# Optimization experiments

Measured on AMD Instinct MI355X. Metric: run time of the kernel, lower is better.

The kernel has to match this reference:

```python
import jax, jax.numpy as jnp
import numpy as np

N_NODES = 50000
N_EDGES = 800000
F_IN, F_HID, F_OUT = 1433, 64, 32


def setup_inputs() -> dict:
    key = jax.random.key(0)
    ks = jax.random.split(key, 8)
    x = jax.random.normal(ks[0], (N_NODES, F_IN), dtype=jnp.float32)
    edge_index = jax.random.randint(ks[1], (2, N_EDGES), 0, N_NODES, dtype=jnp.int32)
    s1 = 1.0 / np.sqrt(F_IN)
    s2 = 1.0 / np.sqrt(F_HID)
    W1_l = jax.random.normal(ks[2], (F_IN, F_HID), dtype=jnp.float32) * s1
    W1_r = jax.random.normal(ks[3], (F_IN, F_HID), dtype=jnp.float32) * s1
    b1 = jnp.zeros((F_HID,), dtype=jnp.float32)
    W2_l = jax.random.normal(ks[4], (F_HID, F_OUT), dtype=jnp.float32) * s2
    W2_r = jax.random.normal(ks[5], (F_HID, F_OUT), dtype=jnp.float32) * s2
    b2 = jnp.zeros((F_OUT,), dtype=jnp.float32)
    return {"x": x, "edge_index": edge_index, "W1_l": W1_l, "b1": b1,
            "W1_r": W1_r, "W2_l": W2_l, "b2": b2, "W2_r": W2_r}


def sage_conv(x, src, dst, W_l, b_l, W_r, num_nodes):
    # PyG SAGEConv: out = lin_l(mean_{j in N(i)} x_j) + lin_r(x_i)
    # lin_l is linear, so project first then aggregate (saves E x F_in gather).
    msg = x @ W_l                                   # [N, F_out]
    agg = jax.ops.segment_sum(msg[src], dst, num_segments=num_nodes)  # [N, F_out]
    deg = jax.ops.segment_sum(jnp.ones_like(src, dtype=x.dtype), dst,
                              num_segments=num_nodes)                 # [N]
    agg = jnp.where(deg[:, None] > 0, agg / jnp.maximum(deg, 1.0)[:, None], 0.0)
    return agg + b_l + x @ W_r


def reference(x, edge_index, W1_l, b1, W1_r, W2_l, b2, W2_r):
    src, dst = edge_index[0], edge_index[1]
    n = x.shape[0]
    h = sage_conv(x, src, dst, W1_l, b1, W1_r, n)   # [N, 64]  (no activation between convs)
    h = sage_conv(h, src, dst, W2_l, b2, W2_r, n)   # [N, 32]
    h = jax.nn.relu(h)
    # dropout p=0.5 is identity in eval mode
    return jax.nn.log_softmax(h, axis=1)
```

## Files before the change

kernel.cpp:

```cpp
#include <hip/hip_runtime.h>
#include <hip/hip_bf16.h>
#include <cstdint>
#include <cstddef>


#define N_NODES 50000
#define N_EDGES 800000
#define F_IN    1433
#define KP      1472
#define NCH     6
#define DMAX    64

typedef __attribute__((ext_vector_type(8))) short bf16x8;
typedef __attribute__((ext_vector_type(4))) float f32x4;

static constexpr size_t OFF_H1PRE = 0;
static constexpr size_t OFF_H1    = OFF_H1PRE + 25600000;
static constexpr size_t OFF_M2    = OFF_H1    + 12800000;
static constexpr size_t OFF_CUR   = OFF_M2    + 12800000;
static constexpr size_t OFF_ESRC  = OFF_CUR   + 200000;
static constexpr size_t OFF_WT    = OFF_ESRC  + 12800000;

__device__ inline ushort f2bf(float f) {
  union { float f; uint32_t u; } v; v.f = f;
  uint32_t u = v.u + 0x7FFFu + ((v.u >> 16) & 1u);
  return (ushort)(u >> 16);
}

__device__ __forceinline__ void gload_lds16(const void* g, void* l) {
  __builtin_amdgcn_global_load_lds(
      (const __attribute__((address_space(1))) void*)g,
      (__attribute__((address_space(3))) void*)l, 16, 0, 0);
}

__global__ __launch_bounds__(256) void k_zero_cur(int* __restrict__ cur) {
  int i = blockIdx.x * 256 + threadIdx.x;
  if (i < N_NODES) cur[i] = 0;
}

__global__ __launch_bounds__(256) void k_prep_w(const float* __restrict__ Wl,
                                                const float* __restrict__ Wr,
                                                ushort* __restrict__ Wt) {
  const int c = blockIdx.x;
  const int k = blockIdx.y * 256 + threadIdx.x;
  if (k >= KP) return;
  float v = 0.f;
  if (k < F_IN) v = (c < 64) ? Wl[k * 64 + c] : Wr[k * 64 + (c - 64)];
  Wt[(size_t)c * KP + k] = f2bf(v);
}

__global__ __launch_bounds__(256) void k_gemm1c(const float* __restrict__ x,
                                                const ushort* __restrict__ Wt,
                                                float* __restrict__ h1pre) {
  __shared__ __align__(16) ushort As[4][32 * 64];
  __shared__ __align__(16) ushort Bs[4][128 * 64];
  const int t    = threadIdx.x;
  const int lane = t & 63;
  const int w    = t >> 6;
  const int wr   = w >> 1;
  const int wc   = w & 1;
  const int row0 = blockIdx.x * 32;

  const int ar = t >> 3;
  const int aq = t & 7;
  const size_t abase = (size_t)(row0 + ar) * F_IN + aq * 8;
  const size_t LIM   = (size_t)N_NODES * F_IN - 4;
  const int aoff = ar * 64;
  const int asw  = (aq ^ (ar & 7)) * 8;

  const int lr = lane >> 3, lt = lane & 7;
  const ushort* b_src[4];
  ushort* b_dst[4];
#pragma unroll
  for (int j = 0; j < 4; ++j) {
    int r = (w * 4 + j) * 8 + lr;
    b_src[j] = Wt + (size_t)r * KP + (lt ^ (r & 7)) * 8;
    b_dst[j] = (ushort*)&Bs[0][(w * 4 + j) * 512];
  }

  f32x4 acc[4] = {};
  f32x4 av[4][2];

#define LOADA_CHUNK(kbase)                                          \
  do {                                                              \
    _Pragma("unroll")                                               \
    for (int s = 0; s < 4; ++s) {                                   \
      size_t i0 = abase + (size_t)(kbase) + s * 64;                 \
      size_t i1 = i0 + 4;                                           \
      if (i0 > LIM) i0 = LIM;                                       \
      if (i1 > LIM) i1 = LIM;                                       \
      __builtin_memcpy(&av[s][0], x + i0, 16);                      \
      __builtin_memcpy(&av[s][1], x + i1, 16);                      \
    }                                                               \
  } while (0)

  LOADA_CHUNK(0);

  for (int c = 0; c < NCH; ++c) {
    const int kbase = c * 256;
    const int nsub = (c < 5) ? 4 : 3;
#pragma unroll
    for (int s = 0; s < 4; ++s) {
      if (s < nsub) {
        bf16x8 w0;
#pragma unroll
        for (int e = 0; e < 4; ++e) {
          w0[e]     = (short)f2bf(av[s][0][e]);
          w0[4 + e] = (short)f2bf(av[s][1][e]);
        }
        *(bf16x8*)&As[s][aoff + asw] = w0;
      }
    }
#pragma unroll
    for (int s = 0; s < 4; ++s) {
      if (s < nsub) {
#pragma unroll
        for (int j = 0; j < 4; ++j)
          gload_lds16(b_src[j] + kbase + s * 64, b_dst[j] + (size_t)s * (128 * 64));
      }
    }
    __syncthreads();
    if (c + 1 < NCH) LOADA_CHUNK(kbase + 256);
    const int nks = (c < 5) ? 8 : 6;
#pragma unroll
    for (int kk = 0; kk < 8; ++kk) {
      if (kk < nks) {
        const int sub = kk >> 1;
        const int sbase = (kk & 1) * 4 + (lane >> 4);
        bf16x8 a, b[4];
        {
          int r = wr * 16 + (lane & 15);
          int s2 = sbase ^ (r & 7);
          a = *(const bf16x8*)&As[sub][r * 64 + s2 * 8];
        }
#pragma unroll
        for (int n = 0; n < 4; ++n) {
          int r = wc * 64 + n * 16 + (lane & 15);
          int s2 = sbase ^ (r & 7);
          b[n] = *(const bf16x8*)&Bs[sub][r * 64 + s2 * 8];
        }
#pragma unroll
        for (int n = 0; n < 4; ++n)
          acc[n] = __builtin_amdgcn_mfma_f32_16x16x32_bf16(a, b[n], acc[n], 0, 0, 0);
      }
    }
    __syncthreads();
  }
#undef LOADA_CHUNK

  {
    int rbase = row0 + wr * 16 + (lane >> 4) * 4;
#pragma unroll
    for (int n = 0; n < 4; ++n) {
      int col = wc * 64 + n * 16 + (lane & 15);
#pragma unroll
      for (int r = 0; r < 4; ++r) {
        int grow = rbase + r;
        if (grow < N_NODES) h1pre[(size_t)grow * 128 + col] = acc[n][r];
      }
    }
  }
}

__global__ void k_fill_pad(const int* __restrict__ ei, int* __restrict__ cur,
                           int* __restrict__ esrc) {
  int e = blockIdx.x * blockDim.x + threadIdx.x;
  if (e < N_EDGES) {
    int s = ei[e];
    int d = ei[N_EDGES + e];
    int slot = atomicAdd(&cur[d], 1);
    if (slot < DMAX) esrc[(size_t)d * DMAX + slot] = s;
  }
}

__global__ __launch_bounds__(256) void k_agg1(const float* __restrict__ h1pre,
                                              const int* __restrict__ cur,
                                              const int* __restrict__ esrc,
                                              const float* __restrict__ b1,
                                              float* __restrict__ h1) {
  const int lane = threadIdx.x & 63;
  const int d = blockIdx.x * 4 + (threadIdx.x >> 6);
  if (d >= N_NODES) return;
  int dg = cur[d]; if (dg > DMAX) dg = DMAX;
  const size_t base = (size_t)d * DMAX;
  float a0 = 0.f, a1 = 0.f, a2 = 0.f, a3 = 0.f;
  float a4 = 0.f, a5 = 0.f, a6 = 0.f, a7 = 0.f;
  int j = 0;
  for (; j + 8 <= dg; j += 8) {
    int s0 = esrc[base + j],     s1 = esrc[base + j + 1];
    int s2 = esrc[base + j + 2], s3 = esrc[base + j + 3];
    int s4 = esrc[base + j + 4], s5 = esrc[base + j + 5];
    int s6 = esrc[base + j + 6], s7 = esrc[base + j + 7];
    a0 += h1pre[(size_t)s0 * 128 + lane];
    a1 += h1pre[(size_t)s1 * 128 + lane];
    a2 += h1pre[(size_t)s2 * 128 + lane];
    a3 += h1pre[(size_t)s3 * 128 + lane];
    a4 += h1pre[(size_t)s4 * 128 + lane];
    a5 += h1pre[(size_t)s5 * 128 + lane];
    a6 += h1pre[(size_t)s6 * 128 + lane];
    a7 += h1pre[(size_t)s7 * 128 + lane];
  }
  for (; j + 4 <= dg; j += 4) {
    int s0 = esrc[base + j],     s1 = esrc[base + j + 1];
    int s2 = esrc[base + j + 2], s3 = esrc[base + j + 3];
    a0 += h1pre[(size_t)s0 * 128 + lane];
    a1 += h1pre[(size_t)s1 * 128 + lane];
    a2 += h1pre[(size_t)s2 * 128 + lane];
    a3 += h1pre[(size_t)s3 * 128 + lane];
  }
  for (; j < dg; ++j) a0 += h1pre[(size_t)esrc[base + j] * 128 + lane];
  float acc = ((a0 + a1) + (a2 + a3)) + ((a4 + a5) + (a6 + a7));
  const float inv = (dg > 0) ? 1.f / (float)dg : 0.f;
  h1[(size_t)d * 64 + lane] = acc * inv + b1[lane] + h1pre[(size_t)d * 128 + 64 + lane];
}

__global__ __launch_bounds__(256) void k_gemm2(const float* __restrict__ h1,
                                               const float* __restrict__ W2l,
                                               const float* __restrict__ W2r,
                                               float* __restrict__ m2) {
  __shared__ __align__(16) float Ws[64][68];
  __shared__ __align__(16) float Hs[32][68];
  const int t = threadIdx.x;
#pragma unroll
  for (int i = 0; i < 16; ++i) {
    int idx = t + 256 * i;
    int k = idx >> 6, c = idx & 63;
    Ws[k][c] = (c < 32) ? W2l[k * 32 + c] : W2r[k * 32 + (c - 32)];
  }
  const int r0 = blockIdx.x * 32;
#pragma unroll
  for (int i = 0; i < 8; ++i) {
    int idx = t + 256 * i;
    int r = idx >> 6, c = idx & 63;
    int gr = r0 + r;
    Hs[r][c] = (gr < N_NODES) ? h1[(size_t)gr * 64 + c] : 0.f;
  }
  __syncthreads();
  const int rl = t >> 3;
  const int c0 = (t & 7) * 8;
  float acc[8] = {};
#pragma unroll 8
  for (int k = 0; k < 64; ++k) {
    float hv = Hs[rl][k];
#pragma unroll
    for (int j = 0; j < 8; ++j) acc[j] = fmaf(hv, Ws[k][c0 + j], acc[j]);
  }
  const int gr = r0 + rl;
  if (gr < N_NODES) {
    *(float4*)(&m2[(size_t)gr * 64 + c0])     = make_float4(acc[0], acc[1], acc[2], acc[3]);
    *(float4*)(&m2[(size_t)gr * 64 + c0 + 4]) = make_float4(acc[4], acc[5], acc[6], acc[7]);
  }
}

__global__ __launch_bounds__(256) void k_agg2(const float* __restrict__ m2,
                                              const int* __restrict__ cur,
                                              const int* __restrict__ esrc,
                                              const float* __restrict__ b2,
                                              float* __restrict__ out) {
  const int lane = threadIdx.x & 63;
  const int half = lane >> 5;
  const int f = lane & 31;
  const int d = blockIdx.x * 8 + ((threadIdx.x >> 6) << 1) + half;
  int dg = cur[d]; if (dg > DMAX) dg = DMAX;
  const size_t base = (size_t)d * DMAX;
  float a0 = 0.f, a1 = 0.f, a2 = 0.f, a3 = 0.f;
  float a4 = 0.f, a5 = 0.f, a6 = 0.f, a7 = 0.f;
  int j = 0;
  for (; j + 8 <= dg; j += 8) {
    int s0 = esrc[base + j],     s1 = esrc[base + j + 1];
    int s2 = esrc[base + j + 2], s3 = esrc[base + j + 3];
    int s4 = esrc[base + j + 4], s5 = esrc[base + j + 5];
    int s6 = esrc[base + j + 6], s7 = esrc[base + j + 7];
    a0 += m2[(size_t)s0 * 64 + f];
    a1 += m2[(size_t)s1 * 64 + f];
    a2 += m2[(size_t)s2 * 64 + f];
    a3 += m2[(size_t)s3 * 64 + f];
    a4 += m2[(size_t)s4 * 64 + f];
    a5 += m2[(size_t)s5 * 64 + f];
    a6 += m2[(size_t)s6 * 64 + f];
    a7 += m2[(size_t)s7 * 64 + f];
  }
  for (; j + 4 <= dg; j += 4) {
    int s0 = esrc[base + j],     s1 = esrc[base + j + 1];
    int s2 = esrc[base + j + 2], s3 = esrc[base + j + 3];
    a0 += m2[(size_t)s0 * 64 + f];
    a1 += m2[(size_t)s1 * 64 + f];
    a2 += m2[(size_t)s2 * 64 + f];
    a3 += m2[(size_t)s3 * 64 + f];
  }
  for (; j < dg; ++j) a0 += m2[(size_t)esrc[base + j] * 64 + f];
  float acc = ((a0 + a1) + (a2 + a3)) + ((a4 + a5) + (a6 + a7));
  const float inv = (dg > 0) ? 1.f / (float)dg : 0.f;
  float v = acc * inv + b2[f] + m2[(size_t)d * 64 + 32 + f];
  v = fmaxf(v, 0.f);
  float m = v;
#pragma unroll
  for (int o = 16; o > 0; o >>= 1) m = fmaxf(m, __shfl_xor(m, o, 32));
  float e = expf(v - m);
  float sum = e;
#pragma unroll
  for (int o = 16; o > 0; o >>= 1) sum += __shfl_xor(sum, o, 32);
  out[(size_t)d * 32 + f] = v - m - logf(sum);
}

extern "C" void kernel_launch(void* const* d_in, const int* in_sizes, int n_in,
                              void* d_out, int out_size, void* d_ws, size_t ws_size,
                              hipStream_t stream) {
  const float* x   = (const float*)d_in[0];
  const int*   ei  = (const int*)d_in[1];
  const float* W1l = (const float*)d_in[2];
  const float* b1  = (const float*)d_in[3];
  const float* W1r = (const float*)d_in[4];
  const float* W2l = (const float*)d_in[5];
  const float* b2  = (const float*)d_in[6];
  const float* W2r = (const float*)d_in[7];
  float* out = (float*)d_out;

  char* ws = (char*)d_ws;
  float*  h1pre = (float*)(ws + OFF_H1PRE);
  float*  h1    = (float*)(ws + OFF_H1);
  float*  m2    = (float*)(ws + OFF_M2);
  int*    cur   = (int*)(ws + OFF_CUR);
  int*    esrc  = (int*)(ws + OFF_ESRC);
  ushort* Wt    = (ushort*)(ws + OFF_WT);

  k_zero_cur<<<(N_NODES + 255) / 256, 256, 0, stream>>>(cur);

  {
    dim3 g(128, (KP + 255) / 256);
    k_prep_w<<<g, 256, 0, stream>>>(W1l, W1r, Wt);
  }
  k_gemm1c<<<(N_NODES + 31) / 32, 256, 0, stream>>>(x, Wt, h1pre);

  k_fill_pad<<<(N_EDGES + 255) / 256, 256, 0, stream>>>(ei, cur, esrc);

  k_agg1<<<N_NODES / 4, 256, 0, stream>>>(h1pre, cur, esrc, b1, h1);
  k_gemm2<<<(N_NODES + 31) / 32, 256, 0, stream>>>(h1, W2l, W2r, m2);
  k_agg2<<<N_NODES / 8, 256, 0, stream>>>(m2, cur, esrc, b2, out);
}
```

Before: 220.4 us.

## Fuse layer-1 aggregation with layer-2 GEMM via bf16 MFMA; merge init kernels

Result: faster. 203.5 us (-7.7%).

```diff
diff --git a/kernel.cpp b/kernel.cpp
--- a/kernel.cpp
+++ b/kernel.cpp
@@ -15,8 +15,7 @@
 typedef __attribute__((ext_vector_type(4))) float f32x4;
 
 static constexpr size_t OFF_H1PRE = 0;
-static constexpr size_t OFF_H1    = OFF_H1PRE + 25600000;
-static constexpr size_t OFF_M2    = OFF_H1    + 12800000;
+static constexpr size_t OFF_M2    = OFF_H1PRE + 25600000;
 static constexpr size_t OFF_CUR   = OFF_M2    + 12800000;
 static constexpr size_t OFF_ESRC  = OFF_CUR   + 200000;
 static constexpr size_t OFF_WT    = OFF_ESRC  + 12800000;
@@ -33,20 +32,22 @@
       (__attribute__((address_space(3))) void*)l, 16, 0, 0);
 }
 
-__global__ __launch_bounds__(256) void k_zero_cur(int* __restrict__ cur) {
-  int i = blockIdx.x * 256 + threadIdx.x;
-  if (i < N_NODES) cur[i] = 0;
-}
-
-__global__ __launch_bounds__(256) void k_prep_w(const float* __restrict__ Wl,
-                                                const float* __restrict__ Wr,
-                                                ushort* __restrict__ Wt) {
-  const int c = blockIdx.x;
-  const int k = blockIdx.y * 256 + threadIdx.x;
-  if (k >= KP) return;
-  float v = 0.f;
-  if (k < F_IN) v = (c < 64) ? Wl[k * 64 + c] : Wr[k * 64 + (c - 64)];
-  Wt[(size_t)c * KP + k] = f2bf(v);
+__global__ __launch_bounds__(256) void k_init(const float* __restrict__ Wl,
+                                              const float* __restrict__ Wr,
+                                              ushort* __restrict__ Wt,
+                                              int* __restrict__ cur) {
+  const int bid = blockIdx.x;
+  if (bid < 768) {
+    const int c  = bid & 127;
+    const int k  = (bid >> 7) * 256 + threadIdx.x;
+    if (k >= KP) return;
+    float v = 0.f;
+    if (k < F_IN) v = (c < 64) ? Wl[k * 64 + c] : Wr[k * 64 + (c - 64)];
+    Wt[(size_t)c * KP + k] = f2bf(v);
+  } else {
+    int i = (bid - 768) * 256 + threadIdx.x;
+    if (i < N_NODES) cur[i] = 0;
+  }
 }
 
 __global__ __launch_bounds__(256) void k_gemm1c(const float* __restrict__ x,
@@ -173,82 +174,98 @@
   }
 }
 
-__global__ __launch_bounds__(256) void k_agg1(const float* __restrict__ h1pre,
-                                              const int* __restrict__ cur,
-                                              const int* __restrict__ esrc,
-                                              const float* __restrict__ b1,
-                                              float* __restrict__ h1) {
-  const int lane = threadIdx.x & 63;
-  const int d = blockIdx.x * 4 + (threadIdx.x >> 6);
-  if (d >= N_NODES) return;
-  int dg = cur[d]; if (dg > DMAX) dg = DMAX;
-  const size_t base = (size_t)d * DMAX;
-  float a0 = 0.f, a1 = 0.f, a2 = 0.f, a3 = 0.f;
-  float a4 = 0.f, a5 = 0.f, a6 = 0.f, a7 = 0.f;
-  int j = 0;
-  for (; j + 8 <= dg; j += 8) {
-    int s0 = esrc[base + j],     s1 = esrc[base + j + 1];
-    int s2 = esrc[base + j + 2], s3 = esrc[base + j + 3];
-    int s4 = esrc[base + j + 4], s5 = esrc[base + j + 5];
-    int s6 = esrc[base + j + 6], s7 = esrc[base + j + 7];
-    a0 += h1pre[(size_t)s0 * 128 + lane];
-    a1 += h1pre[(size_t)s1 * 128 + lane];
-    a2 += h1pre[(size_t)s2 * 128 + lane];
-    a3 += h1pre[(size_t)s3 * 128 + lane];
-    a4 += h1pre[(size_t)s4 * 128 + lane];
-    a5 += h1pre[(size_t)s5 * 128 + lane];
-    a6 += h1pre[(size_t)s6 * 128 + lane];
-    a7 += h1pre[(size_t)s7 * 128 + lane];
-  }
-  for (; j + 4 <= dg; j += 4) {
-    int s0 = esrc[base + j],     s1 = esrc[base + j + 1];
-    int s2 = esrc[base + j + 2], s3 = esrc[base + j + 3];
-    a0 += h1pre[(size_t)s0 * 128 + lane];
-    a1 += h1pre[(size_t)s1 * 128 + lane];
-    a2 += h1pre[(size_t)s2 * 128 + lane];
-    a3 += h1pre[(size_t)s3 * 128 + lane];
-  }
-  for (; j < dg; ++j) a0 += h1pre[(size_t)esrc[base + j] * 128 + lane];
-  float acc = ((a0 + a1) + (a2 + a3)) + ((a4 + a5) + (a6 + a7));
-  const float inv = (dg > 0) ? 1.f / (float)dg : 0.f;
-  h1[(size_t)d * 64 + lane] = acc * inv + b1[lane] + h1pre[(size_t)d * 128 + 64 + lane];
-}
-
-__global__ __launch_bounds__(256) void k_gemm2(const float* __restrict__ h1,
-                                               const float* __restrict__ W2l,
-                                               const float* __restrict__ W2r,
-                                               float* __restrict__ m2) {
-  __shared__ __align__(16) float Ws[64][68];
-  __shared__ __align__(16) float Hs[32][68];
+__global__ __launch_bounds__(256) void k_agg1mm(const float* __restrict__ h1pre,
+                                                const int* __restrict__ cur,
+                                                const int* __restrict__ esrc,
+                                                const float* __restrict__ b1,
+                                                const float* __restrict__ W2l,
+                                                const float* __restrict__ W2r,
+                                                float* __restrict__ m2) {
+  __shared__ __align__(16) ushort Hs[32][72];
+  __shared__ __align__(16) ushort Ws[64][72];
   const int t = threadIdx.x;
+  const int lane = t & 63;
+  const int w = t >> 6;
+
 #pragma unroll
   for (int i = 0; i < 16; ++i) {
     int idx = t + 256 * i;
     int k = idx >> 6, c = idx & 63;
-    Ws[k][c] = (c < 32) ? W2l[k * 32 + c] : W2r[k * 32 + (c - 32)];
-  }
-  const int r0 = blockIdx.x * 32;
-#pragma unroll
+    float v = (c < 32) ? W2l[k * 32 + c] : W2r[k * 32 + (c - 32)];
+    Ws[c][k] = f2bf(v);
+  }
+
+  const float bl = b1[lane];
+  const int dbase = blockIdx.x * 32 + w * 8;
+#pragma unroll 1
   for (int i = 0; i < 8; ++i) {
-    int idx = t + 256 * i;
-    int r = idx >> 6, c = idx & 63;
-    int gr = r0 + r;
-    Hs[r][c] = (gr < N_NODES) ? h1[(size_t)gr * 64 + c] : 0.f;
+    const int d = dbase + i;
+    ushort hv = 0;
+    if (d < N_NODES) {
+      int dg = cur[d]; if (dg > DMAX) dg = DMAX;
+      const size_t base = (size_t)d * DMAX;
+      float a0 = 0.f, a1 = 0.f, a2 = 0.f, a3 = 0.f;
+      float a4 = 0.f, a5 = 0.f, a6 = 0.f, a7 = 0.f;
+      int j = 0;
+      for (; j + 8 <= dg; j += 8) {
+        int s0 = esrc[base + j],     s1 = esrc[base + j + 1];
+        int s2 = esrc[base + j + 2], s3 = esrc[base + j + 3];
+        int s4 = esrc[base + j + 4], s5 = esrc[base + j + 5];
+        int s6 = esrc[base + j + 6], s7 = esrc[base + j + 7];
+        a0 += h1pre[(size_t)s0 * 128 + lane];
+        a1 += h1pre[(size_t)s1 * 128 + lane];
+        a2 += h1pre[(size_t)s2 * 128 + lane];
+        a3 += h1pre[(size_t)s3 * 128 + lane];
+        a4 += h1pre[(size_t)s4 * 128 + lane];
+        a5 += h1pre[(size_t)s5 * 128 + lane];
+        a6 += h1pre[(size_t)s6 * 128 + lane];
+        a7 += h1pre[(size_t)s7 * 128 + lane];
+      }
+      for (; j + 4 <= dg; j += 4) {
+        int s0 = esrc[base + j],     s1 = esrc[base + j + 1];
+        int s2 = esrc[base + j + 2], s3 = esrc[base + j + 3];
+        a0 += h1pre[(size_t)s0 * 128 + lane];
+        a1 += h1pre[(size_t)s1 * 128 + lane];
+        a2 += h1pre[(size_t)s2 * 128 + lane];
+        a3 += h1pre[(size_t)s3 * 128 + lane];
+      }
+      for (; j < dg; ++j) a0 += h1pre[(size_t)esrc[base + j] * 128 + lane];
+      float acc = ((a0 + a1) + (a2 + a3)) + ((a4 + a5) + (a6 + a7));
+      const float inv = (dg > 0) ? 1.f / (float)dg : 0.f;
+      float h = acc * inv + bl + h1pre[(size_t)d * 128 + 64 + lane];
+      hv = f2bf(h);
+    }
+    Hs[w * 8 + i][lane] = hv;
   }
   __syncthreads();
-  const int rl = t >> 3;
-  const int c0 = (t & 7) * 8;
-  float acc[8] = {};
-#pragma unroll 8
-  for (int k = 0; k < 64; ++k) {
-    float hv = Hs[rl][k];
-#pragma unroll
-    for (int j = 0; j < 8; ++j) acc[j] = fmaf(hv, Ws[k][c0 + j], acc[j]);
-  }
-  const int gr = r0 + rl;
-  if (gr < N_NODES) {
-    *(float4*)(&m2[(size_t)gr * 64 + c0])     = make_float4(acc[0], acc[1], acc[2], acc[3]);
-    *(float4*)(&m2[(size_t)gr * 64 + c0 + 4]) = make_float4(acc[4], acc[5], acc[6], acc[7]);
+
+  const int wr2 = w >> 1;
+  f32x4 acc2[2] = {};
+#pragma unroll
+  for (int j = 0; j < 2; ++j) {
+    bf16x8 a;
+    {
+      int r = wr2 * 16 + (lane & 15);
+      a = *(const bf16x8*)&Hs[r][j * 32 + (lane >> 4) * 8];
+    }
+#pragma unroll
+    for (int n = 0; n < 2; ++n) {
+      int c = ((w & 1) * 2 + n) * 16 + (lane & 15);
+      bf16x8 b = *(const bf16x8*)&Ws[c][j * 32 + (lane >> 4) * 8];
+      acc2[n] = __builtin_amdgcn_mfma_f32_16x16x32_bf16(a, b, acc2[n], 0, 0, 0);
+    }
+  }
+  {
+    int rbase = blockIdx.x * 32 + wr2 * 16 + (lane >> 4) * 4;
+#pragma unroll
+    for (int n = 0; n < 2; ++n) {
+      int col = ((w & 1) * 2 + n) * 16 + (lane & 15);
+#pragma unroll
+      for (int r = 0; r < 4; ++r) {
+        int grow = rbase + r;
+        if (grow < N_NODES) m2[(size_t)grow * 64 + col] = acc2[n][r];
+      }
+    }
   }
 }
 
@@ -318,23 +335,18 @@
 
   char* ws = (char*)d_ws;
   float*  h1pre = (float*)(ws + OFF_H1PRE);
-  float*  h1    = (float*)(ws + OFF_H1);
   float*  m2    = (float*)(ws + OFF_M2);
   int*    cur   = (int*)(ws + OFF_CUR);
   int*    esrc  = (int*)(ws + OFF_ESRC);
   ushort* Wt    = (ushort*)(ws + OFF_WT);
 
-  k_zero_cur<<<(N_NODES + 255) / 256, 256, 0, stream>>>(cur);
-
-  {
-    dim3 g(128, (KP + 255) / 256);
-    k_prep_w<<<g, 256, 0, stream>>>(W1l, W1r, Wt);
-  }
+  k_init<<<768 + (N_NODES + 255) / 256, 256, 0, stream>>>(W1l, W1r, Wt, cur);
+
   k_gemm1c<<<(N_NODES + 31) / 32, 256, 0, stream>>>(x, Wt, h1pre);
 
   k_fill_pad<<<(N_EDGES + 255) / 256, 256, 0, stream>>>(ei, cur, esrc);
 
-  k_agg1<<<N_NODES / 4, 256, 0, stream>>>(h1pre, cur, esrc, b1, h1);
-  k_gemm2<<<(N_NODES + 31) / 32, 256, 0, stream>>>(h1, W2l, W2r, m2);
+  k_agg1mm<<<(N_NODES + 31) / 32, 256, 0, stream>>>(h1pre, cur, esrc, b1,
+                                                    W2l, W2r, m2);
   k_agg2<<<N_NODES / 8, 256, 0, stream>>>(m2, cur, esrc, b2, out);
 }
```
